# Optimization experiments

Measured on AMD Instinct MI355X. Metric: run time of the kernel, lower is better.

The kernel has to match this reference:

```python
import jax, jax.numpy as jnp
import numpy as np

N = 100000
E = 6400000
IN_CH = 128
HID = 8
HEADS = 2
OUT_CH = 1
NEG_SLOPE = 0.2


def gat_conv(x, src, dst, W, a_src, a_dst, bias, heads, out_ch, concat, n_nodes):
    # x: [N, F_in], W: [F_in, heads*out_ch], a_src/a_dst: [heads, out_ch]
    h = (x @ W).reshape(n_nodes, heads, out_ch)          # [N, H, C]
    alpha_s = jnp.sum(h * a_src[None], axis=-1)          # [N, H]
    alpha_d = jnp.sum(h * a_dst[None], axis=-1)          # [N, H]
    alpha = alpha_s[src] + alpha_d[dst]                  # [E, H]
    alpha = jax.nn.leaky_relu(alpha, NEG_SLOPE)
    # segment softmax over incoming edges of each destination node
    seg_max = jax.ops.segment_max(alpha, dst, num_segments=n_nodes)  # [N, H]
    alpha = jnp.exp(alpha - seg_max[dst])
    denom = jax.ops.segment_sum(alpha, dst, num_segments=n_nodes)    # [N, H]
    alpha = alpha / (denom[dst] + 1e-16)
    msg = h[src] * alpha[..., None]                       # [E, H, C]
    out = jax.ops.segment_sum(msg, dst, num_segments=n_nodes)        # [N, H, C]
    if concat:
        out = out.reshape(n_nodes, heads * out_ch)
    else:
        out = out.mean(axis=1)
    return out + bias


def setup_inputs() -> dict:
    key = jax.random.key(0)
    ks = jax.random.split(key, 12)
    x = jax.random.normal(ks[0], (N, IN_CH), dtype=jnp.float32)
    edge_index = jax.random.randint(ks[1], (2, E), 0, N, dtype=jnp.int64)
    s1 = 1.0 / np.sqrt(IN_CH)
    W1 = jax.random.normal(ks[2], (IN_CH, HEADS * HID), dtype=jnp.float32) * s1
    a_src1 = jax.random.normal(ks[3], (HEADS, HID), dtype=jnp.float32) * (1.0 / np.sqrt(HID))
    a_dst1 = jax.random.normal(ks[4], (HEADS, HID), dtype=jnp.float32) * (1.0 / np.sqrt(HID))
    b1 = jnp.zeros((HEADS * HID,), dtype=jnp.float32)
    s2 = 1.0 / np.sqrt(HEADS * HID)
    W2 = jax.random.normal(ks[5], (HEADS * HID, OUT_CH), dtype=jnp.float32) * s2
    a_src2 = jax.random.normal(ks[6], (1, OUT_CH), dtype=jnp.float32)
    a_dst2 = jax.random.normal(ks[7], (1, OUT_CH), dtype=jnp.float32)
    b2 = jnp.zeros((OUT_CH,), dtype=jnp.float32)
    return {"x": x, "edge_index": edge_index, "W1": W1, "a_src1": a_src1,
            "a_dst1": a_dst1, "b1": b1, "W2": W2, "a_src2": a_src2,
            "a_dst2": a_dst2, "b2": b2}


def reference(x, edge_index, W1, a_src1, a_dst1, b1, W2, a_src2, a_dst2, b2):
    # add self-loops (PyG GATConv default)
    loops = jnp.arange(N, dtype=edge_index.dtype)
    src = jnp.concatenate([edge_index[0], loops])
    dst = jnp.concatenate([edge_index[1], loops])
    h = gat_conv(x, src, dst, W1, a_src1, a_dst1, b1, HEADS, HID, True, N)
    h = jax.nn.relu(h)
    out = gat_conv(h, src, dst, W2, a_src2, a_dst2, b2, 1, OUT_CH, False, N)
    return out
```

## Files before the change

### kernel.cpp

```cpp
#include <hip/hip_runtime.h>
#include <hip/hip_fp16.h>
#include <cstdint>
#include <cstddef>

#define N_NODES 100000
#define E_EDGES 6400000
#define E_TOT   (E_EDGES + N_NODES)
#define IN_CH   128
#define NHID    16
#define BSHIFT  9
#define BSZ     512
#define NBUCK   196
#define CHUNK   6144
#define BCAP    48
#define NCHUNK  ((E_TOT + CHUNK - 1) / CHUNK)

__global__ void k_detect(const int* __restrict__ edge, int* __restrict__ flag) {
    if (blockIdx.x == 0 && threadIdx.x == 0) {
        int odd_or = 0;
        for (int i = 0; i < 64; i++) odd_or |= edge[2 * i + 1];
        flag[0] = (odd_or == 0) ? 1 : 0;
    }
}

__global__ __launch_bounds__(256) void k_gemm1(
        const float* __restrict__ x, const float* __restrict__ W1,
        const float* __restrict__ a_src1, const float* __restrict__ a_dst1,
        __half* __restrict__ h16, float* __restrict__ asrc,
        float* __restrict__ adst) {
    __shared__ __align__(16) float sW[IN_CH * NHID];
    __shared__ __align__(16) float sx[16][132];
    __shared__ float sh[16][17];
    int t = threadIdx.x;
    int r = t >> 4, c = t & 15;
    int row = blockIdx.x * 16 + r;

    const float4* W4 = (const float4*)W1;
    ((float4*)sW)[t] = W4[t];
    ((float4*)sW)[t + 256] = W4[t + 256];

    if (row < N_NODES) {
        const float4* xr = (const float4*)(x + (size_t)row * IN_CH);
        float4 v0 = xr[c];
        float4 v1 = xr[c + 16];
        *(float4*)&sx[r][4 * c] = v0;
        *(float4*)&sx[r][64 + 4 * c] = v1;
    }
    __syncthreads();

    float acc = 0.f;
    if (row < N_NODES) {
        #pragma unroll 16
        for (int k = 0; k < IN_CH; k++) acc = fmaf(sx[r][k], sW[k * NHID + c], acc);
        h16[(size_t)row * NHID + c] = __float2half(acc);
    }
    sh[r][c] = acc;
    __syncthreads();

    if (row < N_NODES && c < 4) {
        int h = c & 1;
        const float* av = (c >= 2) ? a_dst1 : a_src1;
        float s = 0.f;
        #pragma unroll
        for (int q = 0; q < 8; q++) s = fmaf(sh[r][h * 8 + q], av[h * 8 + q], s);
        if (c < 2) asrc[2 * (size_t)row + c] = s;
        else       adst[2 * (size_t)row + (c - 2)] = s;
    }
}

__global__ __launch_bounds__(256) void k_ccount(const int* __restrict__ edge,
                                                const int* __restrict__ flag,
                                                int* __restrict__ ccnt) {
    __shared__ int sc[NBUCK];
    int m64 = flag[0];
    int t = threadIdx.x;
    for (int i = t; i < NBUCK; i += 256) sc[i] = 0;
    __syncthreads();
    size_t c0 = (size_t)blockIdx.x * CHUNK;
    size_t cend = c0 + CHUNK; if (cend > E_TOT) cend = E_TOT;
    size_t ee = (cend < (size_t)E_EDGES) ? cend : (size_t)E_EDGES;

    if (m64) {
        const int4* dp = (const int4*)(edge + 2 * (size_t)E_EDGES);
        for (size_t i = c0 + 2 * t; i < ee; i += 512) {
            int4 v = dp[i >> 1];
            atomicAdd(&sc[v.x >> BSHIFT], 1);
            if (i + 1 < ee) atomicAdd(&sc[v.z >> BSHIFT], 1);
        }
    } else {
        const int4* dp = (const int4*)(edge + (size_t)E_EDGES);
        for (size_t i = c0 + 4 * t; i < ee; i += 1024) {
            int4 v = dp[i >> 2];
            atomicAdd(&sc[v.x >> BSHIFT], 1);
            if (i + 1 < ee) atomicAdd(&sc[v.y >> BSHIFT], 1);
            if (i + 2 < ee) atomicAdd(&sc[v.z >> BSHIFT], 1);
            if (i + 3 < ee) atomicAdd(&sc[v.w >> BSHIFT], 1);
        }
    }
    size_t sl0 = (c0 > (size_t)E_EDGES) ? c0 : (size_t)E_EDGES;
    for (size_t i = sl0 + t; i < cend; i += 256) {
        int d = (int)(i - E_EDGES);
        atomicAdd(&sc[d >> BSHIFT], 1);
    }
    __syncthreads();
    for (int i = t; i < NBUCK; i += 256)
        ccnt[(size_t)blockIdx.x * NBUCK + i] = sc[i];
}

__global__ __launch_bounds__(256) void k_cscan(int* __restrict__ ccnt,
                                               int* __restrict__ bcnt) {
    __shared__ int sd[256];
    __shared__ int carry;
    int b = blockIdx.x, t = threadIdx.x;
    if (t == 0) carry = 0;
    __syncthreads();
    for (int base = 0; base < NCHUNK; base += 256) {
        int c = base + t;
        int v = (c < NCHUNK) ? ccnt[(size_t)c * NBUCK + b] : 0;
        sd[t] = v;
        __syncthreads();
        for (int ofs = 1; ofs < 256; ofs <<= 1) {
            int a = sd[t];
            int bb = (t >= ofs) ? sd[t - ofs] : 0;
            __syncthreads();
            sd[t] = a + bb;
            __syncthreads();
        }
        if (c < NCHUNK) ccnt[(size_t)c * NBUCK + b] = sd[t] - v + carry;
        __syncthreads();
        if (t == 255) carry += sd[255];
        __syncthreads();
    }
    if (t == 0) bcnt[b] = carry;
}

__global__ void k_bscan(const int* __restrict__ bcnt, int* __restrict__ bbase) {
    __shared__ int sd[256];
    int t = threadIdx.x;
    int v = (t < NBUCK) ? bcnt[t] : 0;
    sd[t] = v;
    __syncthreads();
    for (int ofs = 1; ofs < 256; ofs <<= 1) {
        int a = sd[t];
        int b = (t >= ofs) ? sd[t - ofs] : 0;
        __syncthreads();
        sd[t] = a + b;
        __syncthreads();
    }
    if (t < NBUCK) bbase[t] = sd[t] - v;
    if (t == NBUCK) bbase[NBUCK] = sd[NBUCK - 1];
}

__global__ __launch_bounds__(256) void k_bin(const int* __restrict__ edge,
                                             const int* __restrict__ flag,
                                             const int* __restrict__ ccnt,
                                             const int* __restrict__ bbase,
                                             unsigned* __restrict__ staged) {
    __shared__ unsigned lbin[NBUCK][BCAP];
    __shared__ int lcnt[NBUCK];
    __shared__ int lbase[NBUCK];
    int m64 = flag[0];
    int t = threadIdx.x;
    int g = t >> 4, lane = t & 15;

    size_t c0 = (size_t)blockIdx.x * CHUNK;
    if (c0 >= E_TOT) return;
    size_t cend = c0 + CHUNK; if (cend > E_TOT) cend = E_TOT;
    size_t ee = (cend < (size_t)E_EDGES) ? cend : (size_t)E_EDGES;

    for (int i = t; i < NBUCK; i += 256) {
        lcnt[i] = 0;
        lbase[i] = bbase[i] + ccnt[(size_t)blockIdx.x * NBUCK + i];
    }
    __syncthreads();

    auto put = [&](int s, int d) {
        int b = d >> BSHIFT;
        unsigned v = (unsigned)s | ((unsigned)(d & (BSZ - 1)) << 17);
        int idx = atomicAdd(&lcnt[b], 1);
        if (idx < BCAP) lbin[b][idx] = v;
        else            staged[lbase[b] + idx] = v;
    };

    if (m64) {
        const int4* sp = (const int4*)edge;
        const int4* dp = (const int4*)(edge + 2 * (size_t)E_EDGES);
        for (size_t i = c0 + 2 * t; i < ee; i += 512) {
            int4 sv = sp[i >> 1];
            int4 dv = dp[i >> 1];
            put(sv.x, dv.x);
            if (i + 1 < ee) put(sv.z, dv.z);
        }
    } else {
        const int4* sp = (const int4*)edge;
        const int4* dp = (const int4*)(edge + (size_t)E_EDGES);
        for (size_t i = c0 + 4 * t; i < ee; i += 1024) {
            int4 sv = sp[i >> 2];
            int4 dv = dp[i >> 2];
            put(sv.x, dv.x);
            if (i + 1 < ee) put(sv.y, dv.y);
            if (i + 2 < ee) put(sv.z, dv.z);
            if (i + 3 < ee) put(sv.w, dv.w);
        }
    }
    size_t sl0 = (c0 > (size_t)E_EDGES) ? c0 : (size_t)E_EDGES;
    for (size_t i = sl0 + t; i < cend; i += 256) {
        int d = (int)(i - E_EDGES);
        put(d, d);
    }
    __syncthreads();
    for (int b = g; b < NBUCK; b += 16) {
        int n = min(lcnt[b], BCAP);
        if (!n) continue;
        int pos = lbase[b];
        for (int i = lane; i < n; i += 16) staged[pos + i] = lbin[b][i];
    }
}

__global__ __launch_bounds__(1024) void k_sort(const unsigned* __restrict__ staged,
                                               const int* __restrict__ bbase,
                                               const float* __restrict__ asrc,
                                               const float* __restrict__ adst,
                                               uint2* __restrict__ csr8,
                                               int* __restrict__ offs) {
    __shared__ int hist[BSZ];
    __shared__ int histlo[BSZ];
    __shared__ int lcur[BSZ];
    __shared__ float2 sadp[BSZ];
    int bkt = blockIdx.x >> 1, p = blockIdx.x & 1;
    int t = threadIdx.x;
    int beg = bbase[bkt], end = bbase[bkt + 1];
    int mid = beg + ((end - beg + 1) >> 1);
    int dbase = bkt << BSHIFT;

    if (t < BSZ) { hist[t] = 0; histlo[t] = 0; }
    for (int i = t; i < BSZ; i += 1024) {
        int dd = dbase + i;
        sadp[i] = (dd < N_NODES) ? ((const float2*)adst)[dd] : make_float2(0.f, 0.f);
    }
    __syncthreads();
    for (int e = beg + t; e < end; e += 1024) {
        int dl = staged[e] >> 17;
        atomicAdd(&hist[dl], 1);
        if (e < mid) atomicAdd(&histlo[dl], 1);
    }
    __syncthreads();

    int myv = (t < BSZ) ? hist[t] : 0;
    __syncthreads();
    for (int ofs = 1; ofs < BSZ; ofs <<= 1) {
        int a = 0, b = 0;
        if (t < BSZ) { a = hist[t]; b = (t >= ofs) ? hist[t - ofs] : 0; }
        __syncthreads();
        if (t < BSZ) hist[t] = a + b;
        __syncthreads();
    }
    if (t < BSZ) {
        int excl = hist[t] - myv;
        lcur[t] = excl + (p ? histlo[t] : 0);
        if (p == 0) {
            int dd = dbase + t;
            if (dd < N_NODES) offs[dd] = beg + excl;
        }
    }
    if (bkt == NBUCK - 1 && p == 0 && t == 0) offs[N_NODES] = E_TOT;
    __syncthreads();

    int lo = p ? mid : beg;
    int hi = p ? end : mid;
    for (int e = lo + t; e < hi; e += 1024) {
        unsigned v = staged[e];
        int s  = (int)(v & 0x1FFFFu);
        int dl = (int)(v >> 17);
        float2 asp = ((const float2*)asrc)[s];
        float a0 = asp.x + sadp[dl].x; a0 = (a0 > 0.f) ? a0 : 0.2f * a0;
        float a1 = asp.y + sadp[dl].y; a1 = (a1 > 0.f) ? a1 : 0.2f * a1;
        __half2 hp = __floats2half2_rn(__expf(a0), __expf(a1));
        int pos = atomicAdd(&lcur[dl], 1);
        csr8[beg + pos] = make_uint2(*(unsigned*)&hp, (unsigned)s);
    }
}

__global__ __launch_bounds__(256) void k_edge1(
        const int* __restrict__ offs, const uint2* __restrict__ csr8,
        const __half* __restrict__ h16,
        const float* __restrict__ b1, const float* __restrict__ W2,
        float* __restrict__ h2out) {
    __shared__ float sacc[256][9];
    int t = threadIdx.x;
    int lane = t & 15;
    int g = t >> 4;
    int d = blockIdx.x * 16 + g;
    if (d >= N_NODES) return;

    int sub = lane & 1;
    int pr  = lane >> 1;
    int beg = offs[d], end = offs[d + 1];

    float acc[8];
    #pragma unroll
    for (int c = 0; c < 8; c++) acc[c] = 0.f;
    float den = 0.f;

    auto loadslot = [&](int ee, uint2& ps, float4& hv) {
        if (ee < end) {
            ps = csr8[ee];
            hv = *(const float4*)(h16 + (size_t)ps.y * NHID + sub * 8);
        }
    };
    auto consume = [&](const uint2& ps, const float4& hv) {
        __half2 hp = *(const __half2*)&ps.x;
        float pw = sub ? __half2float(hp.y) : __half2float(hp.x);
        den += pw;
        const __half2* hh = (const __half2*)&hv;
        #pragma unroll
        for (int q = 0; q < 4; q++) {
            float2 f = __half22float2(hh[q]);
            acc[2 * q]     = fmaf(pw, f.x, acc[2 * q]);
            acc[2 * q + 1] = fmaf(pw, f.y, acc[2 * q + 1]);
        }
    };

    uint2 psA{}, psB{}, psC{}, psD{}, psE{}, psF{};
    float4 z4 = make_float4(0.f, 0.f, 0.f, 0.f);
    float4 hA = z4, hB = z4, hC = z4, hD = z4, hE = z4, hF = z4;

    int e = beg + pr;
    loadslot(e,      psA, hA);
    loadslot(e + 8,  psB, hB);
    loadslot(e + 16, psC, hC);
    loadslot(e + 24, psD, hD);
    loadslot(e + 32, psE, hE);
    loadslot(e + 40, psF, hF);
    while (true) {
        if (e >= end) break;
        consume(psA, hA); loadslot(e + 48, psA, hA); e += 8;
        if (e >= end) break;
        consume(psB, hB); loadslot(e + 48, psB, hB); e += 8;
        if (e >= end) break;
        consume(psC, hC); loadslot(e + 48, psC, hC); e += 8;
        if (e >= end) break;
        consume(psD, hD); loadslot(e + 48, psD, hD); e += 8;
        if (e >= end) break;
        consume(psE, hE); loadslot(e + 48, psE, hE); e += 8;
        if (e >= end) break;
        consume(psF, hF); loadslot(e + 48, psF, hF); e += 8;
    }
    den += __shfl_xor(den, 2, 64);
    den += __shfl_xor(den, 4, 64);
    den += __shfl_xor(den, 8, 64);
    #pragma unroll
    for (int c = 0; c < 8; c++) sacc[t][c] = acc[c];
    float sum = 0.f;
    int rowb = g * 16 + (lane >> 3);
    int ch = lane & 7;
    #pragma unroll
    for (int pp = 0; pp < 8; pp++) sum += sacc[rowb + 2 * pp][ch];

    int wgbase = t & 0x30;
    float denh = __shfl(den, wgbase | (lane >> 3), 64);

    float o = sum / (denh + 1e-16f) + b1[lane];
    o = (o > 0.f) ? o : 0.f;
    float v = o * W2[lane];
    v += __shfl_xor(v, 1, 64);
    v += __shfl_xor(v, 2, 64);
    v += __shfl_xor(v, 4, 64);
    v += __shfl_xor(v, 8, 64);
    if (lane == 0) h2out[d] = v;
}

__global__ __launch_bounds__(256) void k_edge2(
        const int* __restrict__ offs, const uint2* __restrict__ csr8,
        const float* __restrict__ h2,
        const float* __restrict__ a_src2, const float* __restrict__ a_dst2,
        const float* __restrict__ b2, float* __restrict__ out) {
    int t = threadIdx.x;
    int g = t >> 4, lane = t & 15;
    int d = blockIdx.x * 16 + g;
    if (d >= N_NODES) return;

    float as2 = a_src2[0], ad2 = a_dst2[0];
    float adv = h2[d] * ad2;
    int beg = offs[d], end = offs[d + 1];

    float den = 0.f, acc = 0.f;
    auto ls = [&](int ee, float& hs) { if (ee < end) hs = h2[csr8[ee].y]; };
    auto cs = [&](float hs) {
        float a = fmaf(hs, as2, adv);
        a = (a > 0.f) ? a : 0.2f * a;
        float p = __expf(a);
        den += p;
        acc = fmaf(p, hs, acc);
    };
    float hA = 0.f, hB = 0.f, hC = 0.f, hD = 0.f, hE = 0.f, hF = 0.f;
    int e = beg + lane;
    ls(e, hA); ls(e + 16, hB); ls(e + 32, hC);
    ls(e + 48, hD); ls(e + 64, hE); ls(e + 80, hF);
    while (true) {
        if (e >= end) break;
        cs(hA); ls(e + 96, hA); e += 16;
        if (e >= end) break;
        cs(hB); ls(e + 96, hB); e += 16;
        if (e >= end) break;
        cs(hC); ls(e + 96, hC); e += 16;
        if (e >= end) break;
        cs(hD); ls(e + 96, hD); e += 16;
        if (e >= end) break;
        cs(hE); ls(e + 96, hE); e += 16;
        if (e >= end) break;
        cs(hF); ls(e + 96, hF); e += 16;
    }
    #pragma unroll
    for (int m = 1; m < 16; m <<= 1) {
        den += __shfl_xor(den, m, 64);
        acc += __shfl_xor(acc, m, 64);
    }
    if (lane == 0) out[d] = acc / (den + 1e-16f) + b2[0];
}

extern "C" void kernel_launch(void* const* d_in, const int* in_sizes, int n_in,
                              void* d_out, int out_size, void* d_ws, size_t ws_size,
                              hipStream_t stream) {
    const float* x      = (const float*)d_in[0];
    const int*   edge   = (const int*)  d_in[1];
    const float* W1     = (const float*)d_in[2];
    const float* a_src1 = (const float*)d_in[3];
    const float* a_dst1 = (const float*)d_in[4];
    const float* b1     = (const float*)d_in[5];
    const float* W2     = (const float*)d_in[6];
    const float* a_src2 = (const float*)d_in[7];
    const float* a_dst2 = (const float*)d_in[8];
    const float* b2     = (const float*)d_in[9];

    constexpr size_t A = 256;
    auto al = [](size_t b) { return (b + A - 1) / A * A; };
    char* ws = (char*)d_ws;
    size_t off = 0;
    int*      flag   = (int*)(ws + off);      off += al(256);
    int*      ccnt   = (int*)(ws + off);      off += al((size_t)NCHUNK * NBUCK * 4);
    int*      bcnt   = (int*)(ws + off);      off += al(NBUCK * 4);
    int*      bbase  = (int*)(ws + off);      off += al((NBUCK + 1) * 4);
    unsigned* staged = (unsigned*)(ws + off); off += al((size_t)E_TOT * 4);
    uint2*    csr8   = (uint2*)(ws + off);    off += al((size_t)E_TOT * 8);
    int*      offs   = (int*)(ws + off);      off += al((size_t)(N_NODES + 1) * 4);
    __half*   h16    = (__half*)(ws + off);   off += al((size_t)N_NODES * NHID * 2);
    float*    asrc   = (float*)(ws + off);    off += al((size_t)N_NODES * 2 * 4);
    float*    adst   = (float*)(ws + off);    off += al((size_t)N_NODES * 2 * 4);
    float*    h2     = (float*)(ws + off);    off += al((size_t)N_NODES * 4);
    (void)ws_size; (void)in_sizes; (void)n_in; (void)out_size;

    k_detect<<<1, 64, 0, stream>>>(edge, flag);
    k_gemm1 <<<(N_NODES + 15) / 16, 256, 0, stream>>>(x, W1, a_src1, a_dst1, h16, asrc, adst);
    k_ccount<<<NCHUNK, 256, 0, stream>>>(edge, flag, ccnt);
    k_cscan <<<NBUCK, 256, 0, stream>>>(ccnt, bcnt);
    k_bscan <<<1, 256, 0, stream>>>(bcnt, bbase);
    k_bin   <<<NCHUNK, 256, 0, stream>>>(edge, flag, ccnt, bbase, staged);
    k_sort  <<<NBUCK * 2, 1024, 0, stream>>>(staged, bbase, asrc, adst, csr8, offs);
    k_edge1 <<<(N_NODES + 15) / 16, 256, 0, stream>>>(offs, csr8, h16, b1, W2, h2);
    k_edge2 <<<(N_NODES + 15) / 16, 256, 0, stream>>>(offs, csr8, h2, a_src2, a_dst2, b2,
                                                      (float*)d_out);
}
```

Before: 233.9 us.

## Move layer-1 attention exp from sort into edge1, shrink CSR to int indices

The sort kernel no longer gathers asrc/adst or computes the exp'd attention weights; it writes only 4-byte source indices instead of 8-byte (weight, index) pairs. The edge1 kernel now gathers asrc per edge and computes the leaky-relu and exp inline, and edge2 reads the smaller CSR. This halves CSR write and read traffic but adds an extra random 8-byte gather per edge-lane in edge1, plus per-edge exp work there.

```diff
diff --git a/kernel.cpp b/kernel.cpp
--- a/kernel.cpp
+++ b/kernel.cpp
@@ -219,14 +219,11 @@
 
 __global__ __launch_bounds__(1024) void k_sort(const unsigned* __restrict__ staged,
                                                const int* __restrict__ bbase,
-                                               const float* __restrict__ asrc,
-                                               const float* __restrict__ adst,
-                                               uint2* __restrict__ csr8,
+                                               int* __restrict__ csr,
                                                int* __restrict__ offs) {
     __shared__ int hist[BSZ];
     __shared__ int histlo[BSZ];
     __shared__ int lcur[BSZ];
-    __shared__ float2 sadp[BSZ];
     int bkt = blockIdx.x >> 1, p = blockIdx.x & 1;
     int t = threadIdx.x;
     int beg = bbase[bkt], end = bbase[bkt + 1];
@@ -234,10 +231,6 @@
     int dbase = bkt << BSHIFT;
 
     if (t < BSZ) { hist[t] = 0; histlo[t] = 0; }
-    for (int i = t; i < BSZ; i += 1024) {
-        int dd = dbase + i;
-        sadp[i] = (dd < N_NODES) ? ((const float2*)adst)[dd] : make_float2(0.f, 0.f);
-    }
     __syncthreads();
     for (int e = beg + t; e < end; e += 1024) {
         int dl = staged[e] >> 17;
@@ -270,20 +263,15 @@
     int hi = p ? end : mid;
     for (int e = lo + t; e < hi; e += 1024) {
         unsigned v = staged[e];
-        int s  = (int)(v & 0x1FFFFu);
-        int dl = (int)(v >> 17);
-        float2 asp = ((const float2*)asrc)[s];
-        float a0 = asp.x + sadp[dl].x; a0 = (a0 > 0.f) ? a0 : 0.2f * a0;
-        float a1 = asp.y + sadp[dl].y; a1 = (a1 > 0.f) ? a1 : 0.2f * a1;
-        __half2 hp = __floats2half2_rn(__expf(a0), __expf(a1));
-        int pos = atomicAdd(&lcur[dl], 1);
-        csr8[beg + pos] = make_uint2(*(unsigned*)&hp, (unsigned)s);
+        int pos = atomicAdd(&lcur[v >> 17], 1);
+        csr[beg + pos] = (int)(v & 0x1FFFFu);
     }
 }
 
 __global__ __launch_bounds__(256) void k_edge1(
-        const int* __restrict__ offs, const uint2* __restrict__ csr8,
-        const __half* __restrict__ h16,
+        const int* __restrict__ offs, const int* __restrict__ csr,
+        const __half* __restrict__ h16, const float* __restrict__ asrc,
+        const float* __restrict__ adst,
         const float* __restrict__ b1, const float* __restrict__ W2,
         float* __restrict__ h2out) {
     __shared__ float sacc[256][9];
@@ -295,6 +283,8 @@
 
     int sub = lane & 1;
     int pr  = lane >> 1;
+    float2 adp = ((const float2*)adst)[d];
+    float adpv = sub ? adp.y : adp.x;
     int beg = offs[d], end = offs[d + 1];
 
     float acc[8];
@@ -302,15 +292,17 @@
     for (int c = 0; c < 8; c++) acc[c] = 0.f;
     float den = 0.f;
 
-    auto loadslot = [&](int ee, uint2& ps, float4& hv) {
+    auto loadslot = [&](int ee, float& aspv, float4& hv) {
         if (ee < end) {
-            ps = csr8[ee];
-            hv = *(const float4*)(h16 + (size_t)ps.y * NHID + sub * 8);
+            int s = csr[ee];
+            float2 asp = ((const float2*)asrc)[s];
+            aspv = sub ? asp.y : asp.x;
+            hv = *(const float4*)(h16 + (size_t)s * NHID + sub * 8);
         }
     };
-    auto consume = [&](const uint2& ps, const float4& hv) {
-        __half2 hp = *(const __half2*)&ps.x;
-        float pw = sub ? __half2float(hp.y) : __half2float(hp.x);
+    auto consume = [&](float aspv, const float4& hv) {
+        float a = aspv + adpv; a = (a > 0.f) ? a : 0.2f * a;
+        float pw = __expf(a);
         den += pw;
         const __half2* hh = (const __half2*)&hv;
         #pragma unroll
@@ -321,30 +313,30 @@
         }
     };
 
-    uint2 psA{}, psB{}, psC{}, psD{}, psE{}, psF{};
+    float aA = 0.f, aB = 0.f, aC = 0.f, aD = 0.f, aE = 0.f, aF = 0.f;
     float4 z4 = make_float4(0.f, 0.f, 0.f, 0.f);
     float4 hA = z4, hB = z4, hC = z4, hD = z4, hE = z4, hF = z4;
 
     int e = beg + pr;
-    loadslot(e,      psA, hA);
-    loadslot(e + 8,  psB, hB);
-    loadslot(e + 16, psC, hC);
-    loadslot(e + 24, psD, hD);
-    loadslot(e + 32, psE, hE);
-    loadslot(e + 40, psF, hF);
+    loadslot(e,      aA, hA);
+    loadslot(e + 8,  aB, hB);
+    loadslot(e + 16, aC, hC);
+    loadslot(e + 24, aD, hD);
+    loadslot(e + 32, aE, hE);
+    loadslot(e + 40, aF, hF);
     while (true) {
         if (e >= end) break;
-        consume(psA, hA); loadslot(e + 48, psA, hA); e += 8;
-        if (e >= end) break;
-        consume(psB, hB); loadslot(e + 48, psB, hB); e += 8;
-        if (e >= end) break;
-        consume(psC, hC); loadslot(e + 48, psC, hC); e += 8;
-        if (e >= end) break;
-        consume(psD, hD); loadslot(e + 48, psD, hD); e += 8;
-        if (e >= end) break;
-        consume(psE, hE); loadslot(e + 48, psE, hE); e += 8;
-        if (e >= end) break;
-        consume(psF, hF); loadslot(e + 48, psF, hF); e += 8;
+        consume(aA, hA); loadslot(e + 48, aA, hA); e += 8;
+        if (e >= end) break;
+        consume(aB, hB); loadslot(e + 48, aB, hB); e += 8;
+        if (e >= end) break;
+        consume(aC, hC); loadslot(e + 48, aC, hC); e += 8;
+        if (e >= end) break;
+        consume(aD, hD); loadslot(e + 48, aD, hD); e += 8;
+        if (e >= end) break;
+        consume(aE, hE); loadslot(e + 48, aE, hE); e += 8;
+        if (e >= end) break;
+        consume(aF, hF); loadslot(e + 48, aF, hF); e += 8;
     }
     den += __shfl_xor(den, 2, 64);
     den += __shfl_xor(den, 4, 64);
@@ -371,7 +363,7 @@
 }
 
 __global__ __launch_bounds__(256) void k_edge2(
-        const int* __restrict__ offs, const uint2* __restrict__ csr8,
+        const int* __restrict__ offs, const int* __restrict__ csr,
         const float* __restrict__ h2,
         const float* __restrict__ a_src2, const float* __restrict__ a_dst2,
         const float* __restrict__ b2, float* __restrict__ out) {
@@ -385,7 +377,7 @@
     int beg = offs[d], end = offs[d + 1];
 
     float den = 0.f, acc = 0.f;
-    auto ls = [&](int ee, float& hs) { if (ee < end) hs = h2[csr8[ee].y]; };
+    auto ls = [&](int ee, float& hs) { if (ee < end) hs = h2[csr[ee]]; };
     auto cs = [&](float hs) {
         float a = fmaf(hs, as2, adv);
         a = (a > 0.f) ? a : 0.2f * a;
@@ -442,7 +434,7 @@
     int*      bcnt   = (int*)(ws + off);      off += al(NBUCK * 4);
     int*      bbase  = (int*)(ws + off);      off += al((NBUCK + 1) * 4);
     unsigned* staged = (unsigned*)(ws + off); off += al((size_t)E_TOT * 4);
-    uint2*    csr8   = (uint2*)(ws + off);    off += al((size_t)E_TOT * 8);
+    int*      csr    = (int*)(ws + off);      off += al((size_t)E_TOT * 4);
     int*      offs   = (int*)(ws + off);      off += al((size_t)(N_NODES + 1) * 4);
     __half*   h16    = (__half*)(ws + off);   off += al((size_t)N_NODES * NHID * 2);
     float*    asrc   = (float*)(ws + off);    off += al((size_t)N_NODES * 2 * 4);
@@ -456,8 +448,8 @@
     k_cscan <<<NBUCK, 256, 0, stream>>>(ccnt, bcnt);
     k_bscan <<<1, 256, 0, stream>>>(bcnt, bbase);
     k_bin   <<<NCHUNK, 256, 0, stream>>>(edge, flag, ccnt, bbase, staged);
-    k_sort  <<<NBUCK * 2, 1024, 0, stream>>>(staged, bbase, asrc, adst, csr8, offs);
-    k_edge1 <<<(N_NODES + 15) / 16, 256, 0, stream>>>(offs, csr8, h16, b1, W2, h2);
-    k_edge2 <<<(N_NODES + 15) / 16, 256, 0, stream>>>(offs, csr8, h2, a_src2, a_dst2, b2,
+    k_sort  <<<NBUCK * 2, 1024, 0, stream>>>(staged, bbase, csr, offs);
+    k_edge1 <<<(N_NODES + 15) / 16, 256, 0, stream>>>(offs, csr, h16, asrc, adst, b1, W2, h2);
+    k_edge2 <<<(N_NODES + 15) / 16, 256, 0, stream>>>(offs, csr, h2, a_src2, a_dst2, b2,
                                                       (float*)d_out);
 }
```

Result: no change. 232.3 us (-0.7%).
